# Kernel tuning notes

Hardware: AMD Instinct MI355X
Metric: run time of the kernel (lower is better)

Reference implementation:

```python
import jax, jax.numpy as jnp
import numpy as np

N_NODES = 50000
N_EDGES = 1600000
IN_CH = 128
HIDDEN = 64
OUT_DIM = 64
N_GRAPHS = 64


def setup_inputs() -> dict:
    key = jax.random.key(0)
    ks = jax.random.split(key, 8)
    x = jax.random.normal(ks[0], (N_NODES, IN_CH), dtype=jnp.float32)
    W1 = jax.random.normal(ks[1], (IN_CH, HIDDEN), dtype=jnp.float32) * (1.0 / np.sqrt(IN_CH))
    b1 = jnp.zeros((HIDDEN,), dtype=jnp.float32)
    W2 = jax.random.normal(ks[2], (HIDDEN, HIDDEN), dtype=jnp.float32) * (1.0 / np.sqrt(HIDDEN))
    b2 = jnp.zeros((HIDDEN,), dtype=jnp.float32)
    Wp = jax.random.normal(ks[3], (HIDDEN, OUT_DIM), dtype=jnp.float32) * (1.0 / np.sqrt(HIDDEN))
    bp = jnp.zeros((OUT_DIM,), dtype=jnp.float32)
    edge_index = jax.random.randint(ks[4], (2, N_EDGES), 0, N_NODES, dtype=jnp.int32)
    batch = jnp.sort(jax.random.randint(ks[5], (N_NODES,), 0, N_GRAPHS, dtype=jnp.int32))
    return {"x": x, "W1": W1, "b1": b1, "W2": W2, "b2": b2,
            "Wp": Wp, "bp": bp, "edge_index": edge_index, "batch": batch}


def _gcn_norm(edge_index, num_nodes):
    # add self-loops, then symmetric normalization D^{-1/2} (A+I) D^{-1/2}
    loop = jnp.arange(num_nodes, dtype=edge_index.dtype)
    src = jnp.concatenate([edge_index[0], loop])
    dst = jnp.concatenate([edge_index[1], loop])
    deg = jax.ops.segment_sum(jnp.ones_like(dst, dtype=jnp.float32), dst,
                              num_segments=num_nodes)
    dinv = jnp.where(deg > 0, jax.lax.rsqrt(deg), 0.0)
    norm = dinv[src] * dinv[dst]  # [E+N]
    return src, dst, norm


def _gcn_conv(x, W, b, src, dst, norm, num_nodes):
    h = x @ W                                  # [N, F_out] transform first (F_out small)
    msg = h[src] * norm[:, None]               # gather + scale  [E+N, F_out]
    agg = jax.ops.segment_sum(msg, dst, num_segments=num_nodes)
    return agg + b


def reference(x, W1, b1, W2, b2, Wp, bp, edge_index, batch):
    n = x.shape[0]
    src, dst, norm = _gcn_norm(edge_index, n)
    h = jax.nn.relu(_gcn_conv(x, W1, b1, src, dst, norm, n))
    # dropout: eval mode (identity)
    h = jax.nn.relu(_gcn_conv(h, W2, b2, src, dst, norm, n))
    # global mean pool over graphs in batch
    gsum = jax.ops.segment_sum(h, batch, num_segments=N_GRAPHS)
    cnt = jax.ops.segment_sum(jnp.ones((n,), dtype=h.dtype), batch,
                              num_segments=N_GRAPHS)
    g = gsum / jnp.maximum(cnt, 1.0)[:, None]
    return g @ Wp + bp
```

## Files before the change

kernel.cpp:

```cpp
#include <hip/hip_runtime.h>

#define N_NODES  50000
#define N_EDGESC 1600000
#define N_GRAPHS 64
#define NBUCK    196
#define CHUNK    2048
#define NBLK     782
#define NREP     32

static __device__ __forceinline__ unsigned short f2bf(float f) {
  unsigned u = __float_as_uint(f);
  u += 0x7FFF + ((u >> 16) & 1);
  return (unsigned short)(u >> 16);
}
static __device__ __forceinline__ float bfLo(unsigned u) {
  return __uint_as_float(u << 16);
}
static __device__ __forceinline__ float bfHi(unsigned u) {
  return __uint_as_float(u & 0xFFFF0000u);
}

static __device__ __forceinline__ int lowerb(const int* a, int n, int v) {
  int lo = 0, hi = n;
  while (lo < hi) { int m = (lo + hi) >> 1; if (a[m] < v) lo = m + 1; else hi = m; }
  return lo;
}

__global__ __launch_bounds__(256) void k_hist(const int* __restrict__ dst,
                                              int* __restrict__ bcnt,
                                              float* __restrict__ gsum, int E) {
  __shared__ int hist[NBUCK];
  int t = threadIdx.x, blk = blockIdx.x;
  if (t < NBUCK) hist[t] = 0;
  for (int i = blk * 256 + t; i < NREP * N_GRAPHS * 64; i += NBLK * 256)
    gsum[i] = 0.f;
  __syncthreads();
  int e0 = blk * CHUNK;
#pragma unroll
  for (int i = 0; i < CHUNK; i += 256) {
    int e = e0 + i + t;
    if (e < E) atomicAdd(&hist[dst[e] >> 8], 1);
  }
  __syncthreads();
  if (t < NBUCK) bcnt[(size_t)t * NBLK + blk] = hist[t];
}

__global__ __launch_bounds__(256) void k_cscan(int* __restrict__ bcnt,
                                               int* __restrict__ btot) {
  __shared__ int sm[256];
  int b = blockIdx.x, t = threadIdx.x;
  int* p = bcnt + (size_t)b * NBLK;
  int carry = 0;
  for (int tile = 0; tile < (NBLK + 255) / 256; ++tile) {
    int idx = tile * 256 + t;
    int v = (idx < NBLK) ? p[idx] : 0;
    sm[t] = v;
    __syncthreads();
    for (int o = 1; o < 256; o <<= 1) {
      int add = (t >= o) ? sm[t - o] : 0;
      __syncthreads();
      sm[t] += add;
      __syncthreads();
    }
    int incl = sm[t];
    int total = sm[255];
    if (idx < NBLK) p[idx] = incl - v + carry;
    carry += total;
    __syncthreads();
  }
  if (t == 0) btot[b] = carry;
}

__global__ __launch_bounds__(256) void k_scatter(const int* __restrict__ src,
                                                 const int* __restrict__ dst,
                                                 const int* __restrict__ bcnt,
                                                 const int* __restrict__ btot,
                                                 unsigned* __restrict__ bbuf, int E) {
  __shared__ int base[NBUCK], cur[NBUCK], sm[256];
  int t = threadIdx.x, blk = blockIdx.x;
  int v = (t < NBUCK) ? btot[t] : 0;
  sm[t] = v;
  __syncthreads();
  for (int o = 1; o < 256; o <<= 1) {
    int add = (t >= o) ? sm[t - o] : 0;
    __syncthreads();
    sm[t] += add;
    __syncthreads();
  }
  if (t < NBUCK) {
    base[t] = (sm[t] - v) + bcnt[(size_t)t * NBLK + blk];
    cur[t] = 0;
  }
  __syncthreads();
  int e0 = blk * CHUNK;
#pragma unroll
  for (int i = 0; i < CHUNK; i += 256) {
    int e = e0 + i + t;
    if (e < E) {
      int d = dst[e], b = d >> 8;
      int pos = base[b] + atomicAdd(&cur[b], 1);
      bbuf[pos] = ((unsigned)(d & 255) << 24) | (unsigned)src[e];
    }
  }
}

__global__ __launch_bounds__(512) void k_bsort(const unsigned* __restrict__ bbuf,
                                               const int* __restrict__ btot,
                                               int* __restrict__ csr,
                                               int* __restrict__ row_off,
                                               float* __restrict__ dinv) {
  __shared__ int hist[256], off[256], cur[256], sm[256];
  int b = blockIdx.x, t = threadIdx.x;
  if (t < 256) {
    int v = (t < NBUCK) ? btot[t] : 0;
    sm[t] = v;
    hist[t] = 0; cur[t] = 0;
  }
  __syncthreads();
  for (int o = 1; o < 256; o <<= 1) {
    int add = 0;
    if (t < 256 && t >= o) add = sm[t - o];
    __syncthreads();
    if (t < 256) sm[t] += add;
    __syncthreads();
  }
  int gb = (b > 0) ? sm[b - 1] : 0;
  int cnt = btot[b];
  const unsigned* bp = bbuf + gb;
  for (int i = t; i < cnt; i += 512) atomicAdd(&hist[bp[i] >> 24], 1);
  __syncthreads();
  if (t < 256) off[t] = hist[t];
  __syncthreads();
  for (int o = 1; o < 256; o <<= 1) {
    int add = 0;
    if (t < 256 && t >= o) add = off[t - o];
    __syncthreads();
    if (t < 256) off[t] += add;
    __syncthreads();
  }
  if (t < 256) {
    int excl = off[t] - hist[t];
    off[t] = excl;
    int idx = (b << 8) + t;
    if (idx <= N_NODES) row_off[idx] = gb + excl;
    if (idx < N_NODES)  dinv[idx] = rsqrtf((float)(hist[t] + 1));
  }
  __syncthreads();
  for (int i = t; i < cnt; i += 512) {
    unsigned v = bp[i];
    int ld = v >> 24;
    int pos = atomicAdd(&cur[ld], 1);
    csr[gb + off[ld] + pos] = (int)(v & 0xFFFFFFu);
  }
}

template <int K>
__global__ __launch_bounds__(256) void k_gemm(const float* __restrict__ x,
                                              const float* __restrict__ W,
                                              const float* __restrict__ dinv,
                                              unsigned short* __restrict__ out, int N) {
  constexpr int KS = 64;
  constexpr int KP = KS + 4;
  __shared__ float xs[64 * KP];
  __shared__ float Wl[KS * 64];
  const int t = threadIdx.x;
  const int lane = t & 63;
  const int w = t >> 6;
  const int n0 = blockIdx.x * 64;

  float acc[16];
#pragma unroll
  for (int j = 0; j < 16; ++j) acc[j] = 0.f;

  for (int h = 0; h < K / KS; ++h) {
#pragma unroll
    for (int i = 0; i < KS * 16 / 256; ++i) {
      int li = i * 256 + t;
      float4 v = reinterpret_cast<const float4*>(W + h * KS * 64)[li];
      *reinterpret_cast<float4*>(Wl + li * 4) = v;
    }
#pragma unroll
    for (int i = 0; i < 64 * (KS / 4) / 256; ++i) {
      int li = i * 256 + t;
      int row = li / (KS / 4), c4 = li % (KS / 4);
      int node = n0 + row;
      float4 v = make_float4(0.f, 0.f, 0.f, 0.f);
      if (node < N) v = reinterpret_cast<const float4*>(x + (size_t)node * K + h * KS)[c4];
      *reinterpret_cast<float4*>(xs + row * KP + c4 * 4) = v;
    }
    __syncthreads();

    const float* xr = xs + lane * KP;
    const float* wq = Wl + w * 16;
#pragma unroll 4
    for (int kp = 0; kp < KS / 4; ++kp) {
      float4 xv = *reinterpret_cast<const float4*>(xr + kp * 4);
#pragma unroll
      for (int q = 0; q < 4; ++q) {
        int k = kp * 4 + q;
        float xq = (q == 0) ? xv.x : (q == 1) ? xv.y : (q == 2) ? xv.z : xv.w;
        const float* wk = wq + k * 64;
        float4 w0 = *reinterpret_cast<const float4*>(wk);
        float4 w1 = *reinterpret_cast<const float4*>(wk + 4);
        float4 w2 = *reinterpret_cast<const float4*>(wk + 8);
        float4 w3 = *reinterpret_cast<const float4*>(wk + 12);
        acc[ 0] = fmaf(xq, w0.x, acc[ 0]);
        acc[ 1] = fmaf(xq, w0.y, acc[ 1]);
        acc[ 2] = fmaf(xq, w0.z, acc[ 2]);
        acc[ 3] = fmaf(xq, w0.w, acc[ 3]);
        acc[ 4] = fmaf(xq, w1.x, acc[ 4]);
        acc[ 5] = fmaf(xq, w1.y, acc[ 5]);
        acc[ 6] = fmaf(xq, w1.z, acc[ 6]);
        acc[ 7] = fmaf(xq, w1.w, acc[ 7]);
        acc[ 8] = fmaf(xq, w2.x, acc[ 8]);
        acc[ 9] = fmaf(xq, w2.y, acc[ 9]);
        acc[10] = fmaf(xq, w2.z, acc[10]);
        acc[11] = fmaf(xq, w2.w, acc[11]);
        acc[12] = fmaf(xq, w3.x, acc[12]);
        acc[13] = fmaf(xq, w3.y, acc[13]);
        acc[14] = fmaf(xq, w3.z, acc[14]);
        acc[15] = fmaf(xq, w3.w, acc[15]);
      }
    }
    __syncthreads();
  }

  int node = n0 + lane;
  if (node < N) {
    float dv = dinv[node];
    unsigned pk[8];
#pragma unroll
    for (int j = 0; j < 8; ++j) {
      unsigned lo = f2bf(acc[2 * j] * dv);
      unsigned hi = f2bf(acc[2 * j + 1] * dv);
      pk[j] = lo | (hi << 16);
    }
    unsigned* op = reinterpret_cast<unsigned*>(out + (size_t)node * 64 + w * 16);
    *reinterpret_cast<uint4*>(op)     = make_uint4(pk[0], pk[1], pk[2], pk[3]);
    *reinterpret_cast<uint4*>(op + 4) = make_uint4(pk[4], pk[5], pk[6], pk[7]);
  }
}

static __device__ __forceinline__ void gather_row(const uint4* __restrict__ hsq,
                                                  const int* __restrict__ csr,
                                                  int i, int s0, int s1,
                                                  int slot, int pos, float a[8]) {
  {
    uint4 sv = hsq[(((unsigned)i) << 3) + pos];
    if (slot == 0) {
      a[0] = bfLo(sv.x); a[1] = bfHi(sv.x); a[2] = bfLo(sv.y); a[3] = bfHi(sv.y);
      a[4] = bfLo(sv.z); a[5] = bfHi(sv.z); a[6] = bfLo(sv.w); a[7] = bfHi(sv.w);
    } else {
#pragma unroll
      for (int k = 0; k < 8; ++k) a[k] = 0.f;
    }
  }
  int j = s0;
  for (; j + 32 <= s1; j += 32) {
    int idx[4];
#pragma unroll
    for (int q = 0; q < 4; ++q) idx[q] = csr[j + 8 * q + slot];
    uint4 v[4];
#pragma unroll
    for (int q = 0; q < 4; ++q)
      v[q] = hsq[(((unsigned)idx[q]) << 3) + pos];
#pragma unroll
    for (int q = 0; q < 4; ++q) {
      a[0] += bfLo(v[q].x); a[1] += bfHi(v[q].x);
      a[2] += bfLo(v[q].y); a[3] += bfHi(v[q].y);
      a[4] += bfLo(v[q].z); a[5] += bfHi(v[q].z);
      a[6] += bfLo(v[q].w); a[7] += bfHi(v[q].w);
    }
  }
  if (j < s1) {
    int idx[4];
    bool ok[4];
#pragma unroll
    for (int q = 0; q < 4; ++q) {
      int e = j + 8 * q + slot;
      ok[q] = e < s1;
      idx[q] = csr[min(e, s1 - 1)];
    }
    uint4 v[4];
#pragma unroll
    for (int q = 0; q < 4; ++q)
      v[q] = hsq[(((unsigned)idx[q]) << 3) + pos];
#pragma unroll
    for (int q = 0; q < 4; ++q) {
      if (ok[q]) {
        a[0] += bfLo(v[q].x); a[1] += bfHi(v[q].x);
        a[2] += bfLo(v[q].y); a[3] += bfHi(v[q].y);
        a[4] += bfLo(v[q].z); a[5] += bfHi(v[q].z);
        a[6] += bfLo(v[q].w); a[7] += bfHi(v[q].w);
      }
    }
  }
#pragma unroll
  for (int k = 0; k < 8; ++k) {
    a[k] += __shfl_xor(a[k], 8);
    a[k] += __shfl_xor(a[k], 16);
    a[k] += __shfl_xor(a[k], 32);
  }
}

__global__ __launch_bounds__(256) void k_gather_w2(const unsigned short* __restrict__ hs,
                                                   const int* __restrict__ row_off,
                                                   const int* __restrict__ csr,
                                                   const float* __restrict__ dinv,
                                                   const float* __restrict__ b1,
                                                   const float* __restrict__ W2,
                                                   unsigned short* __restrict__ out2,
                                                   int N) {
  __shared__ float w2l[64 * 65];
  const int t = threadIdx.x;
  const int lane = t & 63;
  const int slot = lane >> 3;
  const int pos  = lane & 7;
  if (t < 64) {
#pragma unroll
    for (int m = 0; m < 8; ++m) {
      const float* gp = W2 + (pos * 8 + m) * 64 + slot * 8;
      float4 wA = *reinterpret_cast<const float4*>(gp);
      float4 wB = *reinterpret_cast<const float4*>(gp + 4);
      float* dp = w2l + lane * 65 + m * 8;
      *reinterpret_cast<float4*>(dp) = wA;
      *reinterpret_cast<float4*>(dp + 4) = wB;
    }
  }
  __syncthreads();

  int wid = blockIdx.x * 4 + (t >> 6);
  int stride = gridDim.x * 4;
  const uint4* hsq = reinterpret_cast<const uint4*>(hs);
  float4 bA = reinterpret_cast<const float4*>(b1)[pos * 2];
  float4 bB = reinterpret_cast<const float4*>(b1)[pos * 2 + 1];
  const float* wl = w2l + lane * 65;

  for (int i = wid; i < N; i += stride) {
    float a[8];
    gather_row(hsq, csr, i, row_off[i], row_off[i + 1], slot, pos, a);
    float dv = dinv[i];
    float h1[8];
    h1[0] = fmaxf(fmaf(a[0], dv, bA.x), 0.f);
    h1[1] = fmaxf(fmaf(a[1], dv, bA.y), 0.f);
    h1[2] = fmaxf(fmaf(a[2], dv, bA.z), 0.f);
    h1[3] = fmaxf(fmaf(a[3], dv, bA.w), 0.f);
    h1[4] = fmaxf(fmaf(a[4], dv, bB.x), 0.f);
    h1[5] = fmaxf(fmaf(a[5], dv, bB.y), 0.f);
    h1[6] = fmaxf(fmaf(a[6], dv, bB.z), 0.f);
    h1[7] = fmaxf(fmaf(a[7], dv, bB.w), 0.f);
    float p[8];
#pragma unroll
    for (int j = 0; j < 8; ++j) p[j] = 0.f;
#pragma unroll
    for (int m = 0; m < 8; ++m) {
      float4 wA = *reinterpret_cast<const float4*>(wl + m * 8);
      float4 wB = *reinterpret_cast<const float4*>(wl + m * 8 + 4);
      p[0] = fmaf(h1[m], wA.x, p[0]);
      p[1] = fmaf(h1[m], wA.y, p[1]);
      p[2] = fmaf(h1[m], wA.z, p[2]);
      p[3] = fmaf(h1[m], wA.w, p[3]);
      p[4] = fmaf(h1[m], wB.x, p[4]);
      p[5] = fmaf(h1[m], wB.y, p[5]);
      p[6] = fmaf(h1[m], wB.z, p[6]);
      p[7] = fmaf(h1[m], wB.w, p[7]);
    }
#pragma unroll
    for (int j = 0; j < 8; ++j) {
      p[j] += __shfl_xor(p[j], 1);
      p[j] += __shfl_xor(p[j], 2);
      p[j] += __shfl_xor(p[j], 4);
    }
    if (pos == 0) {
      unsigned pk[4];
#pragma unroll
      for (int q = 0; q < 4; ++q) {
        unsigned lo = f2bf(p[2 * q] * dv);
        unsigned hi = f2bf(p[2 * q + 1] * dv);
        pk[q] = lo | (hi << 16);
      }
      *reinterpret_cast<uint4*>(out2 + (((size_t)i) << 6) + slot * 8) =
          make_uint4(pk[0], pk[1], pk[2], pk[3]);
    }
  }
}

__global__ __launch_bounds__(256) void k_gather_pool(const unsigned short* __restrict__ hs,
                                                     const int* __restrict__ row_off,
                                                     const int* __restrict__ csr,
                                                     const float* __restrict__ dinv,
                                                     const float* __restrict__ b2,
                                                     const int* __restrict__ batch,
                                                     float* __restrict__ gsum, int N) {
  const int t = threadIdx.x;
  const int lane = t & 63;
  const int slot = lane >> 3;
  const int pos  = lane & 7;
  const int NPW = 8;
  int wid = blockIdx.x * 4 + (t >> 6);
  int base = wid * NPW;
  if (base >= N) return;
  int end = min(base + NPW, N);
  int rep = wid & (NREP - 1);
  const uint4* hsq = reinterpret_cast<const uint4*>(hs);
  float4 bA = reinterpret_cast<const float4*>(b2)[pos * 2];
  float4 bB = reinterpret_cast<const float4*>(b2)[pos * 2 + 1];
  const int srcl = ((lane & 7) << 3) | (lane >> 3);

  float gacc[8];
#pragma unroll
  for (int j = 0; j < 8; ++j) gacc[j] = 0.f;
  int gprev = batch[base];

  for (int i = base; i < end; ++i) {
    float a[8];
    gather_row(hsq, csr, i, row_off[i], row_off[i + 1], slot, pos, a);
    float dv = dinv[i];
    int g = batch[i];
    if (g != gprev) {
      float v = 0.f;
#pragma unroll
      for (int j = 0; j < 8; ++j) {
        float tv = __shfl(gacc[j], srcl);
        if ((lane & 7) == j) v = tv;
      }
      atomicAdd(&gsum[(rep * N_GRAPHS + gprev) * 64 + lane], v);
#pragma unroll
      for (int j = 0; j < 8; ++j) gacc[j] = 0.f;
      gprev = g;
    }
    gacc[0] += fmaxf(fmaf(a[0], dv, bA.x), 0.f);
    gacc[1] += fmaxf(fmaf(a[1], dv, bA.y), 0.f);
    gacc[2] += fmaxf(fmaf(a[2], dv, bA.z), 0.f);
    gacc[3] += fmaxf(fmaf(a[3], dv, bA.w), 0.f);
    gacc[4] += fmaxf(fmaf(a[4], dv, bB.x), 0.f);
    gacc[5] += fmaxf(fmaf(a[5], dv, bB.y), 0.f);
    gacc[6] += fmaxf(fmaf(a[6], dv, bB.z), 0.f);
    gacc[7] += fmaxf(fmaf(a[7], dv, bB.w), 0.f);
  }
  {
    float v = 0.f;
#pragma unroll
    for (int j = 0; j < 8; ++j) {
      float tv = __shfl(gacc[j], srcl);
      if ((lane & 7) == j) v = tv;
    }
    atomicAdd(&gsum[(rep * N_GRAPHS + gprev) * 64 + lane], v);
  }
}

__global__ void k_final(const float* __restrict__ gsum, const int* __restrict__ batch,
                        const float* __restrict__ Wp, const float* __restrict__ bp,
                        float* __restrict__ out, int N) {
  __shared__ int lb[5];
  __shared__ float gs[4][64];
  int t = threadIdx.x;
  int g0 = blockIdx.x * 4;
  if (t < 5) lb[t] = lowerb(batch, N, g0 + t);
  {
    int gl = t >> 6, k = t & 63;
    float s = 0.f;
#pragma unroll
    for (int r = 0; r < NREP; ++r)
      s += gsum[(r * N_GRAPHS + g0 + gl) * 64 + k];
    gs[gl][k] = s;
  }
  __syncthreads();
  int idx = blockIdx.x * 256 + t;
  int o = idx & 63, gl = (idx >> 6) & 3;
  float cinv = 1.0f / fmaxf((float)(lb[gl + 1] - lb[gl]), 1.0f);
  float acc = 0.f;
#pragma unroll
  for (int k = 0; k < 64; ++k) acc += gs[gl][k] * Wp[k * 64 + o];
  out[idx] = fmaf(acc, cinv, bp[o]);
}

extern "C" void kernel_launch(void* const* d_in, const int* in_sizes, int n_in,
                              void* d_out, int out_size, void* d_ws, size_t ws_size,
                              hipStream_t stream) {
  const float* x    = (const float*)d_in[0];
  const float* W1   = (const float*)d_in[1];
  const float* b1   = (const float*)d_in[2];
  const float* W2   = (const float*)d_in[3];
  const float* b2   = (const float*)d_in[4];
  const float* Wp   = (const float*)d_in[5];
  const float* bp   = (const float*)d_in[6];
  const int*   ei   = (const int*)d_in[7];
  const int*   batch= (const int*)d_in[8];
  float* out = (float*)d_out;

  const int N = N_NODES, E = N_EDGESC;
  const int* src  = ei;
  const int* dstp = ei + E;

  char* wsb = (char*)d_ws;
  size_t o = 0;
  auto alloc = [&](size_t bytes) -> void* {
    void* p = wsb + o;
    o = (o + bytes + 255) & ~(size_t)255;
    return p;
  };
  int*      bcnt   = (int*)alloc((size_t)NBUCK * NBLK * 4);
  int*      btot   = (int*)alloc(NBUCK * 4);
  unsigned* bbuf   = (unsigned*)alloc((size_t)E * 4);
  int*      row_off= (int*)alloc((size_t)(N + 1) * 4);
  int*      csr    = (int*)alloc((size_t)E * 4);
  float*    dinv   = (float*)alloc((size_t)N * 4);
  unsigned short* bufA = (unsigned short*)alloc((size_t)N * 64 * 2);
  unsigned short* bufB = (unsigned short*)alloc((size_t)N * 64 * 2);
  float*    gsum   = (float*)alloc((size_t)NREP * N_GRAPHS * 64 * 4);

  int gN64 = (N + 63) / 64;
  int gPool = (N + 31) / 32;

  k_hist<<<NBLK, 256, 0, stream>>>(dstp, bcnt, gsum, E);
  k_cscan<<<NBUCK, 256, 0, stream>>>(bcnt, btot);
  k_scatter<<<NBLK, 256, 0, stream>>>(src, dstp, bcnt, btot, bbuf, E);
  k_bsort<<<NBUCK, 512, 0, stream>>>(bbuf, btot, csr, row_off, dinv);

  k_gemm<128><<<gN64, 256, 0, stream>>>(x, W1, dinv, bufA, N);
  k_gather_w2<<<2048, 256, 0, stream>>>(bufA, row_off, csr, dinv, b1, W2, bufB, N);
  k_gather_pool<<<gPool, 256, 0, stream>>>(bufB, row_off, csr, dinv, b2, batch, gsum, N);
  k_final<<<16, 256, 0, stream>>>(gsum, batch, Wp, bp, out, N);
}
```

Baseline: 165.2 us.

## Batch 8 nodes per wave in gather_w2 and shrink gather tail loop

```diff
diff --git a/kernel.cpp b/kernel.cpp
--- a/kernel.cpp
+++ b/kernel.cpp
@@ -272,27 +272,16 @@
       a[6] += bfLo(v[q].w); a[7] += bfHi(v[q].w);
     }
   }
-  if (j < s1) {
-    int idx[4];
-    bool ok[4];
-#pragma unroll
-    for (int q = 0; q < 4; ++q) {
-      int e = j + 8 * q + slot;
-      ok[q] = e < s1;
-      idx[q] = csr[min(e, s1 - 1)];
-    }
-    uint4 v[4];
-#pragma unroll
-    for (int q = 0; q < 4; ++q)
-      v[q] = hsq[(((unsigned)idx[q]) << 3) + pos];
-#pragma unroll
-    for (int q = 0; q < 4; ++q) {
-      if (ok[q]) {
-        a[0] += bfLo(v[q].x); a[1] += bfHi(v[q].x);
-        a[2] += bfLo(v[q].y); a[3] += bfHi(v[q].y);
-        a[4] += bfLo(v[q].z); a[5] += bfHi(v[q].z);
-        a[6] += bfLo(v[q].w); a[7] += bfHi(v[q].w);
-      }
+  for (; j < s1; j += 8) {
+    int e = j + slot;
+    bool ok = e < s1;
+    int idx = csr[min(e, s1 - 1)];
+    uint4 v = hsq[(((unsigned)idx) << 3) + pos];
+    if (ok) {
+      a[0] += bfLo(v.x); a[1] += bfHi(v.x);
+      a[2] += bfLo(v.y); a[3] += bfHi(v.y);
+      a[4] += bfLo(v.z); a[5] += bfHi(v.z);
+      a[6] += bfLo(v.w); a[7] += bfHi(v.w);
     }
   }
 #pragma unroll
@@ -311,78 +300,73 @@
                                                    const float* __restrict__ W2,
                                                    unsigned short* __restrict__ out2,
                                                    int N) {
-  __shared__ float w2l[64 * 65];
+  __shared__ float w2l[64 * 64];
   const int t = threadIdx.x;
   const int lane = t & 63;
   const int slot = lane >> 3;
   const int pos  = lane & 7;
-  if (t < 64) {
-#pragma unroll
-    for (int m = 0; m < 8; ++m) {
-      const float* gp = W2 + (pos * 8 + m) * 64 + slot * 8;
-      float4 wA = *reinterpret_cast<const float4*>(gp);
-      float4 wB = *reinterpret_cast<const float4*>(gp + 4);
-      float* dp = w2l + lane * 65 + m * 8;
-      *reinterpret_cast<float4*>(dp) = wA;
-      *reinterpret_cast<float4*>(dp + 4) = wB;
-    }
-  }
-  __syncthreads();
-
-  int wid = blockIdx.x * 4 + (t >> 6);
-  int stride = gridDim.x * 4;
+#pragma unroll
+  for (int i = 0; i < 4; ++i) {
+    int li = i * 256 + t;
+    reinterpret_cast<float4*>(w2l)[li] = reinterpret_cast<const float4*>(W2)[li];
+  }
+  __syncthreads();
+
+  int n0 = (blockIdx.x * 4 + (t >> 6)) * 8;
+  if (n0 >= N) return;
   const uint4* hsq = reinterpret_cast<const uint4*>(hs);
   float4 bA = reinterpret_cast<const float4*>(b1)[pos * 2];
   float4 bB = reinterpret_cast<const float4*>(b1)[pos * 2 + 1];
-  const float* wl = w2l + lane * 65;
-
-  for (int i = wid; i < N; i += stride) {
+
+  float h[8];
+#pragma unroll
+  for (int j = 0; j < 8; ++j) h[j] = 0.f;
+
+  for (int i = 0; i < 8; ++i) {
+    int node = n0 + i;
     float a[8];
-    gather_row(hsq, csr, i, row_off[i], row_off[i + 1], slot, pos, a);
-    float dv = dinv[i];
-    float h1[8];
-    h1[0] = fmaxf(fmaf(a[0], dv, bA.x), 0.f);
-    h1[1] = fmaxf(fmaf(a[1], dv, bA.y), 0.f);
-    h1[2] = fmaxf(fmaf(a[2], dv, bA.z), 0.f);
-    h1[3] = fmaxf(fmaf(a[3], dv, bA.w), 0.f);
-    h1[4] = fmaxf(fmaf(a[4], dv, bB.x), 0.f);
-    h1[5] = fmaxf(fmaf(a[5], dv, bB.y), 0.f);
-    h1[6] = fmaxf(fmaf(a[6], dv, bB.z), 0.f);
-    h1[7] = fmaxf(fmaf(a[7], dv, bB.w), 0.f);
-    float p[8];
-#pragma unroll
-    for (int j = 0; j < 8; ++j) p[j] = 0.f;
-#pragma unroll
-    for (int m = 0; m < 8; ++m) {
-      float4 wA = *reinterpret_cast<const float4*>(wl + m * 8);
-      float4 wB = *reinterpret_cast<const float4*>(wl + m * 8 + 4);
-      p[0] = fmaf(h1[m], wA.x, p[0]);
-      p[1] = fmaf(h1[m], wA.y, p[1]);
-      p[2] = fmaf(h1[m], wA.z, p[2]);
-      p[3] = fmaf(h1[m], wA.w, p[3]);
-      p[4] = fmaf(h1[m], wB.x, p[4]);
-      p[5] = fmaf(h1[m], wB.y, p[5]);
-      p[6] = fmaf(h1[m], wB.z, p[6]);
-      p[7] = fmaf(h1[m], wB.w, p[7]);
-    }
-#pragma unroll
-    for (int j = 0; j < 8; ++j) {
-      p[j] += __shfl_xor(p[j], 1);
-      p[j] += __shfl_xor(p[j], 2);
-      p[j] += __shfl_xor(p[j], 4);
-    }
-    if (pos == 0) {
-      unsigned pk[4];
-#pragma unroll
-      for (int q = 0; q < 4; ++q) {
-        unsigned lo = f2bf(p[2 * q] * dv);
-        unsigned hi = f2bf(p[2 * q + 1] * dv);
-        pk[q] = lo | (hi << 16);
-      }
-      *reinterpret_cast<uint4*>(out2 + (((size_t)i) << 6) + slot * 8) =
-          make_uint4(pk[0], pk[1], pk[2], pk[3]);
-    }
-  }
+    gather_row(hsq, csr, node, row_off[node], row_off[node + 1], slot, pos, a);
+    float dv = dinv[node];
+    bool keep = (slot == i);
+    h[0] = keep ? fmaxf(fmaf(a[0], dv, bA.x), 0.f) : h[0];
+    h[1] = keep ? fmaxf(fmaf(a[1], dv, bA.y), 0.f) : h[1];
+    h[2] = keep ? fmaxf(fmaf(a[2], dv, bA.z), 0.f) : h[2];
+    h[3] = keep ? fmaxf(fmaf(a[3], dv, bA.w), 0.f) : h[3];
+    h[4] = keep ? fmaxf(fmaf(a[4], dv, bB.x), 0.f) : h[4];
+    h[5] = keep ? fmaxf(fmaf(a[5], dv, bB.y), 0.f) : h[5];
+    h[6] = keep ? fmaxf(fmaf(a[6], dv, bB.z), 0.f) : h[6];
+    h[7] = keep ? fmaxf(fmaf(a[7], dv, bB.w), 0.f) : h[7];
+  }
+
+  float p[8];
+#pragma unroll
+  for (int j = 0; j < 8; ++j) p[j] = 0.f;
+#pragma unroll
+  for (int k = 0; k < 64; ++k) {
+    float h1k = __shfl(h[k & 7], (slot << 3) | (k >> 3));
+    const float* wk = w2l + k * 64 + pos * 8;
+    float4 wA = *reinterpret_cast<const float4*>(wk);
+    float4 wB = *reinterpret_cast<const float4*>(wk + 4);
+    p[0] = fmaf(h1k, wA.x, p[0]);
+    p[1] = fmaf(h1k, wA.y, p[1]);
+    p[2] = fmaf(h1k, wA.z, p[2]);
+    p[3] = fmaf(h1k, wA.w, p[3]);
+    p[4] = fmaf(h1k, wB.x, p[4]);
+    p[5] = fmaf(h1k, wB.y, p[5]);
+    p[6] = fmaf(h1k, wB.z, p[6]);
+    p[7] = fmaf(h1k, wB.w, p[7]);
+  }
+  int node = n0 + slot;
+  float dvs = dinv[node];
+  unsigned pk[4];
+#pragma unroll
+  for (int q = 0; q < 4; ++q) {
+    unsigned lo = f2bf(p[2 * q] * dvs);
+    unsigned hi = f2bf(p[2 * q + 1] * dvs);
+    pk[q] = lo | (hi << 16);
+  }
+  *reinterpret_cast<uint4*>(out2 + (((size_t)node) << 6) + pos * 8) =
+      make_uint4(pk[0], pk[1], pk[2], pk[3]);
 }
 
 __global__ __launch_bounds__(256) void k_gather_pool(const unsigned short* __restrict__ hs,
@@ -396,7 +380,7 @@
   const int lane = t & 63;
   const int slot = lane >> 3;
   const int pos  = lane & 7;
-  const int NPW = 8;
+  const int NPW = 4;
   int wid = blockIdx.x * 4 + (t >> 6);
   int base = wid * NPW;
   if (base >= N) return;
@@ -511,7 +495,8 @@
   float*    gsum   = (float*)alloc((size_t)NREP * N_GRAPHS * 64 * 4);
 
   int gN64 = (N + 63) / 64;
-  int gPool = (N + 31) / 32;
+  int gW2  = (N + 31) / 32;
+  int gPool = (N + 15) / 16;
 
   k_hist<<<NBLK, 256, 0, stream>>>(dstp, bcnt, gsum, E);
   k_cscan<<<NBUCK, 256, 0, stream>>>(bcnt, btot);
@@ -519,7 +504,7 @@
   k_bsort<<<NBUCK, 512, 0, stream>>>(bbuf, btot, csr, row_off, dinv);
 
   k_gemm<128><<<gN64, 256, 0, stream>>>(x, W1, dinv, bufA, N);
-  k_gather_w2<<<2048, 256, 0, stream>>>(bufA, row_off, csr, dinv, b1, W2, bufB, N);
+  k_gather_w2<<<gW2, 256, 0, stream>>>(bufA, row_off, csr, dinv, b1, W2, bufB, N);
   k_gather_pool<<<gPool, 256, 0, stream>>>(bufB, row_off, csr, dinv, b2, batch, gsum, N);
   k_final<<<16, 256, 0, stream>>>(gsum, batch, Wp, bp, out, N);
 }
```

Measured after the change: 170.9 us. 1.03x slower.
